# Kernel tuning notes

Hardware: AMD Instinct MI355X
Metric: run time of the kernel (lower is better)

Reference implementation:

```python
import jax, jax.numpy as jnp
import numpy as np

B, N, C = 8, 1024, 1024
H = 16
D = C // H  # head_dim = 64
SCALE = D ** -0.5


def setup_inputs() -> dict:
    key = jax.random.key(0)
    k1, k2, k3 = jax.random.split(key, 3)
    x = jax.random.normal(k1, (B, N, C), dtype=jnp.float32)
    w_qkv = jax.random.normal(k2, (3 * C, C), dtype=jnp.float32) * (C ** -0.5)
    w_proj = jax.random.normal(k3, (C, C), dtype=jnp.float32) * (C ** -0.5)
    b_proj = jnp.zeros((C,), dtype=jnp.float32)
    return {"x": x, "w_qkv": w_qkv, "w_proj": w_proj, "b_proj": b_proj}


def reference(x, w_qkv, w_proj, b_proj):
    Bx, Nx, Cx = x.shape
    # qkv: [B,N,3C] -> [3,B,H,N,D]
    qkv = jnp.einsum('bnc,oc->bno', x, w_qkv)
    qkv = qkv.reshape(Bx, Nx, 3, H, D).transpose(2, 0, 3, 1, 4)
    q, k, v = qkv[0], qkv[1], qkv[2]
    attn = jnp.einsum('bhnd,bhmd->bhnm', q, k) * SCALE  # [B,H,N,N]
    attn = jax.nn.softmax(attn, axis=-1)
    out = jnp.einsum('bhnm,bhmd->bhnd', attn, v)  # [B,H,N,D]
    out = out.transpose(0, 2, 1, 3).reshape(Bx, Nx, Cx)
    return jnp.einsum('bnc,oc->bno', out, w_proj) + b_proj
```

## Files before the change

### kernel.cpp

```cpp
#include <hip/hip_runtime.h>

typedef _Float16 half8 __attribute__((ext_vector_type(8)));
typedef _Float16 half4v __attribute__((ext_vector_type(4)));
typedef _Float16 half2v __attribute__((ext_vector_type(2)));
typedef float floatx4 __attribute__((ext_vector_type(4)));

#define AS3 __attribute__((address_space(3)))
#define AS1 __attribute__((address_space(1)))

__global__ __launch_bounds__(256) void cvt_f32_f16(const float* __restrict__ in,
                                                   _Float16* __restrict__ out, int n4) {
    int i = blockIdx.x * 256 + threadIdx.x;
    if (i >= n4) return;
    float4 v = ((const float4*)in)[i];
    half4v h = {(_Float16)v.x, (_Float16)v.y, (_Float16)v.z, (_Float16)v.w};
    ((half4v*)out)[i] = h;
}

__global__ __launch_bounds__(256, 3) void gemm_tn(
    const _Float16* __restrict__ A, const _Float16* __restrict__ B,
    _Float16* __restrict__ Ch, int ldc, _Float16* __restrict__ Ch2, int ldc2, int split,
    float* __restrict__ Cf, const float* __restrict__ bias,
    int M, int Nn, int K)
{
    __shared__ _Float16 sA[2][128 * 32];
    __shared__ _Float16 sB[2][128 * 32];
    const int tid  = threadIdx.x;
    const int lane = tid & 63, wave = tid >> 6;
    const int quad = lane >> 4, l16 = lane & 15;
    const int wr = wave >> 1, wc = wave & 1;
    const long m0 = (long)blockIdx.x * 128, n0 = (long)blockIdx.y * 128;

    const int srow = tid >> 2;
    const int sslot = ((tid & 3) ^ ((srow >> 1) & 3)) * 8;
    const int dlo = srow * 32 + sslot;
    const int dhi = (srow + 64) * 32 + sslot;
    const _Float16* gA0 = A + (m0 + srow) * (long)K + (tid & 3) * 8;
    const _Float16* gA1 = A + (m0 + srow + 64) * (long)K + (tid & 3) * 8;
    const _Float16* gB0 = B + (n0 + srow) * (long)K + (tid & 3) * 8;
    const _Float16* gB1 = B + (n0 + srow + 64) * (long)K + (tid & 3) * 8;

    const int swz = (l16 >> 1) & 3;
    const int aoff = ((quad ^ swz) * 8);

    floatx4 acc[4][4] = {};
    const int nk = K >> 5;

    half8 rA0 = *(const half8*)gA0, rA1 = *(const half8*)gA1;
    half8 rB0 = *(const half8*)gB0, rB1 = *(const half8*)gB1;
    *(half8*)&sA[0][dlo] = rA0; *(half8*)&sA[0][dhi] = rA1;
    *(half8*)&sB[0][dlo] = rB0; *(half8*)&sB[0][dhi] = rB1;

    for (int kk = 0; kk < nk; kk++) {
        const int cur = kk & 1;
        __syncthreads();
        const bool more = (kk + 1 < nk);
        if (more) {
            const long k0 = (long)(kk + 1) << 5;
            rA0 = *(const half8*)(gA0 + k0); rA1 = *(const half8*)(gA1 + k0);
            rB0 = *(const half8*)(gB0 + k0); rB1 = *(const half8*)(gB1 + k0);
        }

        const _Float16* cA = &sA[cur][0];
        const _Float16* cB = &sB[cur][0];
        half8 af[4], bf[4];
#pragma unroll
        for (int t = 0; t < 4; t++)
            af[t] = *(const half8*)&cA[(wr * 64 + t * 16 + l16) * 32 + aoff];
#pragma unroll
        for (int t = 0; t < 4; t++)
            bf[t] = *(const half8*)&cB[(wc * 64 + t * 16 + l16) * 32 + aoff];
#pragma unroll
        for (int tm = 0; tm < 4; tm++)
#pragma unroll
            for (int tn = 0; tn < 4; tn++)
                acc[tm][tn] = __builtin_amdgcn_mfma_f32_16x16x32_f16(af[tm], bf[tn], acc[tm][tn], 0, 0, 0);

        if (more) {
            _Float16* nA = &sA[cur ^ 1][0];
            _Float16* nB = &sB[cur ^ 1][0];
            *(half8*)&nA[dlo] = rA0; *(half8*)&nA[dhi] = rA1;
            *(half8*)&nB[dlo] = rB0; *(half8*)&nB[dhi] = rB1;
        }
    }

    const bool useC2 = (Cf == nullptr) && (n0 >= split);
#pragma unroll
    for (int tm = 0; tm < 4; tm++) {
        long row = m0 + wr * 64 + tm * 16 + quad * 4;
#pragma unroll
        for (int tn = 0; tn < 4; tn++) {
            long col = n0 + wc * 64 + tn * 16 + l16;
            float bv = bias ? bias[col] : 0.f;
#pragma unroll
            for (int r = 0; r < 4; r++) {
                float v = acc[tm][tn][r];
                if (Cf)        Cf[(row + r) * (long)Nn + col] = v + bv;
                else if (useC2) Ch2[(row + r) * (long)ldc2 + (col - split)] = (_Float16)v;
                else           Ch[(row + r) * (long)ldc + col] = (_Float16)v;
            }
        }
    }
}

__global__ __launch_bounds__(256) void transpose_v(const _Float16* __restrict__ vh,
                                                   _Float16* __restrict__ vt) {
    const int bh = blockIdx.x;
    const int b = bh >> 4, h = bh & 15;
    const int n0 = blockIdx.y * 64;
    const int d = threadIdx.x & 63;
    const int ng = threadIdx.x >> 6;
#pragma unroll
    for (int i = 0; i < 2; i++) {
        int nb = (ng + 4 * i) * 8;
        half8 vv;
#pragma unroll
        for (int j = 0; j < 8; j++)
            vv[j] = vh[(long)(b * 1024 + n0 + nb + j) * 1024 + h * 64 + d];
        *(half8*)&vt[((long)(bh * 64 + d)) * 1024 + n0 + nb] = vv;
    }
}

#define CSC 0.125f
__global__ __launch_bounds__(256, 4) void flash_attn(const _Float16* __restrict__ qk,
                                                     const _Float16* __restrict__ vt,
                                                     _Float16* __restrict__ out)
{
    const int bh = blockIdx.x, b = bh >> 4, h = bh & 15;
    const int n0 = blockIdx.y * 128;
    const int tid = threadIdx.x, lane = tid & 63, wave = tid >> 6;
    const int quad = lane >> 4, l16 = lane & 15;

    __shared__ _Float16 sK[64 * 72];
    __shared__ _Float16 sVT[64 * 72];
    __shared__ _Float16 sPT[4][32 * 72];

    half8 qf[2][2];
    const _Float16* qbase = qk + (long)(b * 1024 + n0 + wave * 32) * 2048 + h * 64;
#pragma unroll
    for (int t = 0; t < 2; t++)
#pragma unroll
        for (int s = 0; s < 2; s++)
            qf[t][s] = *(const half8*)(qbase + (long)(t * 16 + l16) * 2048 + s * 32 + quad * 8);

    const int srow = tid >> 3, scol8 = (tid & 7) * 8;
    const _Float16* kgb = qk + 1024 + h * 64 + scol8 + (long)(b * 1024 + srow) * 2048;
    const _Float16* vgb = vt + (long)(bh * 64 + srow) * 1024 + scol8;

    float m_[2] = {-1e30f, -1e30f}, l_[2] = {0.f, 0.f};
    floatx4 o[2][4] = {};

    for (int kt = 0; kt < 16; kt++) {
        const int kr0 = kt * 64;
        __syncthreads();
#pragma unroll
        for (int i = 0; i < 2; i++) {
            int r = srow + i * 32;
            *(half8*)&sK[r * 72 + scol8]  = *(const half8*)(kgb + (long)(kr0 + i * 32) * 2048);
            *(half8*)&sVT[r * 72 + scol8] = *(const half8*)(vgb + (long)(i * 32) * 1024 + kr0);
        }
        __syncthreads();

        floatx4 sacc[2][4] = {};
#pragma unroll
        for (int c = 0; c < 4; c++)
#pragma unroll
            for (int s = 0; s < 2; s++) {
                half8 kf = *(const half8*)&sK[(c * 16 + l16) * 72 + s * 32 + quad * 8];
                sacc[0][c] = __builtin_amdgcn_mfma_f32_16x16x32_f16(kf, qf[0][s], sacc[0][c], 0, 0, 0);
                sacc[1][c] = __builtin_amdgcn_mfma_f32_16x16x32_f16(kf, qf[1][s], sacc[1][c], 0, 0, 0);
            }

#pragma unroll
        for (int t = 0; t < 2; t++) {
            float mx = -1e30f;
#pragma unroll
            for (int c = 0; c < 4; c++)
#pragma unroll
                for (int r = 0; r < 4; r++) {
                    float v = sacc[t][c][r] * CSC;
                    sacc[t][c][r] = v;
                    mx = fmaxf(mx, v);
                }
            mx = fmaxf(mx, __shfl_xor(mx, 16));
            mx = fmaxf(mx, __shfl_xor(mx, 32));
            float mn = fmaxf(m_[t], mx);
            float al = __expf(m_[t] - mn);
            m_[t] = mn;
            float rs = 0.f;
#pragma unroll
            for (int c = 0; c < 4; c++)
#pragma unroll
                for (int r = 0; r < 4; r++) {
                    float p = __expf(sacc[t][c][r] - mn);
                    sacc[t][c][r] = p;
                    rs += p;
                }
            rs += __shfl_xor(rs, 16);
            rs += __shfl_xor(rs, 32);
            l_[t] = l_[t] * al + rs;
#pragma unroll
            for (int dt = 0; dt < 4; dt++) o[t][dt] *= al;
#pragma unroll
            for (int c = 0; c < 4; c++) {
                half2v p01 = {(_Float16)sacc[t][c][0], (_Float16)sacc[t][c][1]};
                half2v p23 = {(_Float16)sacc[t][c][2], (_Float16)sacc[t][c][3]};
                *(half2v*)&sPT[wave][(t * 16 + l16) * 72 + c * 16 + quad * 4]     = p01;
                *(half2v*)&sPT[wave][(t * 16 + l16) * 72 + c * 16 + quad * 4 + 2] = p23;
            }
        }

#pragma unroll
        for (int kk = 0; kk < 2; kk++) {
            half8 pf0 = *(const half8*)&sPT[wave][(l16) * 72 + kk * 32 + quad * 8];
            half8 pf1 = *(const half8*)&sPT[wave][(16 + l16) * 72 + kk * 32 + quad * 8];
#pragma unroll
            for (int dt = 0; dt < 4; dt++) {
                half8 vf = *(const half8*)&sVT[(dt * 16 + l16) * 72 + kk * 32 + quad * 8];
                o[0][dt] = __builtin_amdgcn_mfma_f32_16x16x32_f16(vf, pf0, o[0][dt], 0, 0, 0);
                o[1][dt] = __builtin_amdgcn_mfma_f32_16x16x32_f16(vf, pf1, o[1][dt], 0, 0, 0);
            }
        }
    }

#pragma unroll
    for (int t = 0; t < 2; t++) {
        float inv = 1.f / l_[t];
#pragma unroll
        for (int dt = 0; dt < 4; dt++) {
            floatx4 v = o[t][dt];
            half2v a = {(_Float16)(v[0] * inv), (_Float16)(v[1] * inv)};
            half2v c = {(_Float16)(v[2] * inv), (_Float16)(v[3] * inv)};
            *(half2v*)&sPT[wave][(t * 16 + l16) * 72 + dt * 16 + quad * 4]     = a;
            *(half2v*)&sPT[wave][(t * 16 + l16) * 72 + dt * 16 + quad * 4 + 2] = c;
        }
    }
    __syncthreads();
#pragma unroll
    for (int i = 0; i < 4; i++) {
        int ql = i * 8 + (lane >> 3);
        int c8 = (lane & 7) * 8;
        half8 vv = *(const half8*)&sPT[wave][ql * 72 + c8];
        *(half8*)(out + (long)(b * 1024 + n0 + wave * 32 + ql) * 1024 + h * 64 + c8) = vv;
    }
}

extern "C" void kernel_launch(void* const* d_in, const int* in_sizes, int n_in,
                              void* d_out, int out_size, void* d_ws, size_t ws_size,
                              hipStream_t stream) {
    const float* x      = (const float*)d_in[0];
    const float* w_qkv  = (const float*)d_in[1];
    const float* w_proj = (const float*)d_in[2];
    const float* b_proj = (const float*)d_in[3];

    char* ws = (char*)d_ws;
    _Float16* qkh    = (_Float16*)ws;
    _Float16* vh     = (_Float16*)(ws + 33554432);
    _Float16* xh     = (_Float16*)(ws + 50331648);
    _Float16* wqkvh  = (_Float16*)(ws + 67108864);
    _Float16* wprojh = (_Float16*)(ws + 73400320);
    _Float16* vT     = xh;
    _Float16* attnh  = vh;

    cvt_f32_f16<<<8192, 256, 0, stream>>>(x, xh, 8388608 / 4);
    cvt_f32_f16<<<3072, 256, 0, stream>>>(w_qkv, wqkvh, 3145728 / 4);
    cvt_f32_f16<<<1024, 256, 0, stream>>>(w_proj, wprojh, 1048576 / 4);

    gemm_tn<<<dim3(64, 24), 256, 0, stream>>>(xh, wqkvh, qkh, 2048, vh, 1024, 2048,
                                              nullptr, nullptr, 8192, 3072, 1024);
    transpose_v<<<dim3(128, 16), 256, 0, stream>>>(vh, vT);
    flash_attn<<<dim3(128, 8), 256, 0, stream>>>(qkh, vT, attnh);
    gemm_tn<<<dim3(64, 8), 256, 0, stream>>>(attnh, wprojh, nullptr, 0, nullptr, 0, 1 << 30,
                                             (float*)d_out, b_proj, 8192, 1024, 1024);
}
```

Measured before the change: 265.9 us.

## Load GEMM B fragments directly from global memory and fuse fp32-to-fp16 converts

The GEMM no longer stages the B (weight) tile through shared memory. Each wave loads its four B fragments straight from global memory into registers, prefetching one k-step ahead, which halves LDS traffic and LDS footprint. The cost is redundant global loads: the two waves that share a column block each fetch the same B data, and the per-lane 16-byte reads across rows are less coalesced. Separately, the three conversion kernels are merged into one launch to cut launch overhead.

```diff
diff --git a/kernel.cpp b/kernel.cpp
--- a/kernel.cpp
+++ b/kernel.cpp
@@ -8,13 +8,20 @@
 #define AS3 __attribute__((address_space(3)))
 #define AS1 __attribute__((address_space(1)))
 
-__global__ __launch_bounds__(256) void cvt_f32_f16(const float* __restrict__ in,
-                                                   _Float16* __restrict__ out, int n4) {
-    int i = blockIdx.x * 256 + threadIdx.x;
-    if (i >= n4) return;
-    float4 v = ((const float4*)in)[i];
+__global__ __launch_bounds__(256) void cvt_all(const float* __restrict__ x,
+                                               const float* __restrict__ wq,
+                                               const float* __restrict__ wp,
+                                               _Float16* __restrict__ xh,
+                                               _Float16* __restrict__ wqh,
+                                               _Float16* __restrict__ wph) {
+    long i = (long)blockIdx.x * 256 + threadIdx.x;
+    const float4* src; half4v* dst; long off;
+    if (i < 2097152)      { src = (const float4*)x;  dst = (half4v*)xh;  off = i; }
+    else if (i < 2883584) { src = (const float4*)wq; dst = (half4v*)wqh; off = i - 2097152; }
+    else                  { src = (const float4*)wp; dst = (half4v*)wph; off = i - 2883584; }
+    float4 v = src[off];
     half4v h = {(_Float16)v.x, (_Float16)v.y, (_Float16)v.z, (_Float16)v.w};
-    ((half4v*)out)[i] = h;
+    dst[off] = h;
 }
 
 __global__ __launch_bounds__(256, 3) void gemm_tn(
@@ -24,7 +31,6 @@
     int M, int Nn, int K)
 {
     __shared__ _Float16 sA[2][128 * 32];
-    __shared__ _Float16 sB[2][128 * 32];
     const int tid  = threadIdx.x;
     const int lane = tid & 63, wave = tid >> 6;
     const int quad = lane >> 4, l16 = lane & 15;
@@ -37,8 +43,9 @@
     const int dhi = (srow + 64) * 32 + sslot;
     const _Float16* gA0 = A + (m0 + srow) * (long)K + (tid & 3) * 8;
     const _Float16* gA1 = A + (m0 + srow + 64) * (long)K + (tid & 3) * 8;
-    const _Float16* gB0 = B + (n0 + srow) * (long)K + (tid & 3) * 8;
-    const _Float16* gB1 = B + (n0 + srow + 64) * (long)K + (tid & 3) * 8;
+
+    const _Float16* gB0 = B + (n0 + wc * 64 + l16) * (long)K + quad * 8;
+    const _Float16* gBf[4] = {gB0, gB0 + 16 * (long)K, gB0 + 32 * (long)K, gB0 + 48 * (long)K};
 
     const int swz = (l16 >> 1) & 3;
     const int aoff = ((quad ^ swz) * 8);
@@ -47,30 +54,29 @@
     const int nk = K >> 5;
 
     half8 rA0 = *(const half8*)gA0, rA1 = *(const half8*)gA1;
-    half8 rB0 = *(const half8*)gB0, rB1 = *(const half8*)gB1;
+    half8 bf[4], bn[4];
+#pragma unroll
+    for (int tn = 0; tn < 4; tn++) bf[tn] = *(const half8*)gBf[tn];
     *(half8*)&sA[0][dlo] = rA0; *(half8*)&sA[0][dhi] = rA1;
-    *(half8*)&sB[0][dlo] = rB0; *(half8*)&sB[0][dhi] = rB1;
 
     for (int kk = 0; kk < nk; kk++) {
         const int cur = kk & 1;
         __syncthreads();
         const bool more = (kk + 1 < nk);
         if (more) {
-            const long k0 = (long)(kk + 1) << 5;
-            rA0 = *(const half8*)(gA0 + k0); rA1 = *(const half8*)(gA1 + k0);
-            rB0 = *(const half8*)(gB0 + k0); rB1 = *(const half8*)(gB1 + k0);
+            const long k0n = (long)(kk + 1) << 5;
+            rA0 = *(const half8*)(gA0 + k0n);
+            rA1 = *(const half8*)(gA1 + k0n);
+#pragma unroll
+            for (int tn = 0; tn < 4; tn++) bn[tn] = *(const half8*)(gBf[tn] + k0n);
         }
 
         const _Float16* cA = &sA[cur][0];
-        const _Float16* cB = &sB[cur][0];
-        half8 af[4], bf[4];
+        half8 af[4];
 #pragma unroll
         for (int t = 0; t < 4; t++)
             af[t] = *(const half8*)&cA[(wr * 64 + t * 16 + l16) * 32 + aoff];
 #pragma unroll
-        for (int t = 0; t < 4; t++)
-            bf[t] = *(const half8*)&cB[(wc * 64 + t * 16 + l16) * 32 + aoff];
-#pragma unroll
         for (int tm = 0; tm < 4; tm++)
 #pragma unroll
             for (int tn = 0; tn < 4; tn++)
@@ -78,9 +84,10 @@
 
         if (more) {
             _Float16* nA = &sA[cur ^ 1][0];
-            _Float16* nB = &sB[cur ^ 1][0];
-            *(half8*)&nA[dlo] = rA0; *(half8*)&nA[dhi] = rA1;
-            *(half8*)&nB[dlo] = rB0; *(half8*)&nB[dhi] = rB1;
+            *(half8*)&nA[dlo] = rA0;
+            *(half8*)&nA[dhi] = rA1;
+#pragma unroll
+            for (int tn = 0; tn < 4; tn++) bf[tn] = bn[tn];
         }
     }
 
@@ -262,9 +269,7 @@
     _Float16* vT     = xh;
     _Float16* attnh  = vh;
 
-    cvt_f32_f16<<<8192, 256, 0, stream>>>(x, xh, 8388608 / 4);
-    cvt_f32_f16<<<3072, 256, 0, stream>>>(w_qkv, wqkvh, 3145728 / 4);
-    cvt_f32_f16<<<1024, 256, 0, stream>>>(w_proj, wprojh, 1048576 / 4);
+    cvt_all<<<12288, 256, 0, stream>>>(x, w_qkv, w_proj, xh, wqkvh, wprojh);
 
     gemm_tn<<<dim3(64, 24), 256, 0, stream>>>(xh, wqkvh, qkh, 2048, vh, 1024, 2048,
                                               nullptr, nullptr, 8192, 3072, 1024);
```

Result: slower. 321.1 us (+20.8%).

## Fuse V transpose into QKV GEMM epilogue and merge conversion kernels

Applied to the files above, without the earlier changes.

The QKV GEMM epilogue now writes the V columns directly in transposed [b,h,d,n] layout, which removes the separate transpose_v kernel and its extra read and write of V. The three fp32-to-fp16 conversion launches become one kernel. The GEMM occupancy hint rises from 3 to 4 waves per SIMD, and LDS stores of P and O use 4-wide half vectors instead of pairs. The epilogue's V stores are strided across rows, which may coalesce poorly, and the higher occupancy hint may cause register spills.

```diff
diff --git a/kernel.cpp b/kernel.cpp
--- a/kernel.cpp
+++ b/kernel.cpp
@@ -8,18 +8,25 @@
 #define AS3 __attribute__((address_space(3)))
 #define AS1 __attribute__((address_space(1)))
 
-__global__ __launch_bounds__(256) void cvt_f32_f16(const float* __restrict__ in,
-                                                   _Float16* __restrict__ out, int n4) {
-    int i = blockIdx.x * 256 + threadIdx.x;
-    if (i >= n4) return;
-    float4 v = ((const float4*)in)[i];
+__global__ __launch_bounds__(256) void cvt_all(const float* __restrict__ x,
+                                               const float* __restrict__ wq,
+                                               const float* __restrict__ wp,
+                                               _Float16* __restrict__ xh,
+                                               _Float16* __restrict__ wqh,
+                                               _Float16* __restrict__ wph) {
+    long i = (long)blockIdx.x * 256 + threadIdx.x;
+    const float4* src; half4v* dst; long off;
+    if (i < 2097152)      { src = (const float4*)x;  dst = (half4v*)xh;  off = i; }
+    else if (i < 2883584) { src = (const float4*)wq; dst = (half4v*)wqh; off = i - 2097152; }
+    else                  { src = (const float4*)wp; dst = (half4v*)wph; off = i - 2883584; }
+    float4 v = src[off];
     half4v h = {(_Float16)v.x, (_Float16)v.y, (_Float16)v.z, (_Float16)v.w};
-    ((half4v*)out)[i] = h;
-}
-
-__global__ __launch_bounds__(256, 3) void gemm_tn(
+    dst[off] = h;
+}
+
+__global__ __launch_bounds__(256, 4) void gemm_tn(
     const _Float16* __restrict__ A, const _Float16* __restrict__ B,
-    _Float16* __restrict__ Ch, int ldc, _Float16* __restrict__ Ch2, int ldc2, int split,
+    _Float16* __restrict__ Ch, int ldc, _Float16* __restrict__ Vt, int split,
     float* __restrict__ Cf, const float* __restrict__ bias,
     int M, int Nn, int K)
 {
@@ -84,40 +91,30 @@
         }
     }
 
-    const bool useC2 = (Cf == nullptr) && (n0 >= split);
 #pragma unroll
     for (int tm = 0; tm < 4; tm++) {
         long row = m0 + wr * 64 + tm * 16 + quad * 4;
 #pragma unroll
         for (int tn = 0; tn < 4; tn++) {
             long col = n0 + wc * 64 + tn * 16 + l16;
-            float bv = bias ? bias[col] : 0.f;
-#pragma unroll
-            for (int r = 0; r < 4; r++) {
-                float v = acc[tm][tn][r];
-                if (Cf)        Cf[(row + r) * (long)Nn + col] = v + bv;
-                else if (useC2) Ch2[(row + r) * (long)ldc2 + (col - split)] = (_Float16)v;
-                else           Ch[(row + r) * (long)ldc + col] = (_Float16)v;
-            }
-        }
-    }
-}
-
-__global__ __launch_bounds__(256) void transpose_v(const _Float16* __restrict__ vh,
-                                                   _Float16* __restrict__ vt) {
-    const int bh = blockIdx.x;
-    const int b = bh >> 4, h = bh & 15;
-    const int n0 = blockIdx.y * 64;
-    const int d = threadIdx.x & 63;
-    const int ng = threadIdx.x >> 6;
-#pragma unroll
-    for (int i = 0; i < 2; i++) {
-        int nb = (ng + 4 * i) * 8;
-        half8 vv;
-#pragma unroll
-        for (int j = 0; j < 8; j++)
-            vv[j] = vh[(long)(b * 1024 + n0 + nb + j) * 1024 + h * 64 + d];
-        *(half8*)&vt[((long)(bh * 64 + d)) * 1024 + n0 + nb] = vv;
+            if (Cf) {
+                float bv = bias ? bias[col] : 0.f;
+#pragma unroll
+                for (int r = 0; r < 4; r++)
+                    Cf[(row + r) * (long)Nn + col] = acc[tm][tn][r] + bv;
+            } else if (col >= split) {
+                long cv = col - split;
+                long vrow = ((row >> 10) * 16 + (cv >> 6)) * 64 + (cv & 63);
+                long nn = row & 1023;
+                half4v pv = {(_Float16)acc[tm][tn][0], (_Float16)acc[tm][tn][1],
+                             (_Float16)acc[tm][tn][2], (_Float16)acc[tm][tn][3]};
+                *(half4v*)&Vt[vrow * 1024 + nn] = pv;
+            } else {
+#pragma unroll
+                for (int r = 0; r < 4; r++)
+                    Ch[(row + r) * (long)ldc + col] = (_Float16)acc[tm][tn][r];
+            }
+        }
     }
 }
 
@@ -203,10 +200,9 @@
             for (int dt = 0; dt < 4; dt++) o[t][dt] *= al;
 #pragma unroll
             for (int c = 0; c < 4; c++) {
-                half2v p01 = {(_Float16)sacc[t][c][0], (_Float16)sacc[t][c][1]};
-                half2v p23 = {(_Float16)sacc[t][c][2], (_Float16)sacc[t][c][3]};
-                *(half2v*)&sPT[wave][(t * 16 + l16) * 72 + c * 16 + quad * 4]     = p01;
-                *(half2v*)&sPT[wave][(t * 16 + l16) * 72 + c * 16 + quad * 4 + 2] = p23;
+                half4v p = {(_Float16)sacc[t][c][0], (_Float16)sacc[t][c][1],
+                            (_Float16)sacc[t][c][2], (_Float16)sacc[t][c][3]};
+                *(half4v*)&sPT[wave][(t * 16 + l16) * 72 + c * 16 + quad * 4] = p;
             }
         }
 
@@ -229,10 +225,9 @@
 #pragma unroll
         for (int dt = 0; dt < 4; dt++) {
             floatx4 v = o[t][dt];
-            half2v a = {(_Float16)(v[0] * inv), (_Float16)(v[1] * inv)};
-            half2v c = {(_Float16)(v[2] * inv), (_Float16)(v[3] * inv)};
-            *(half2v*)&sPT[wave][(t * 16 + l16) * 72 + dt * 16 + quad * 4]     = a;
-            *(half2v*)&sPT[wave][(t * 16 + l16) * 72 + dt * 16 + quad * 4 + 2] = c;
+            half4v a = {(_Float16)(v[0] * inv), (_Float16)(v[1] * inv),
+                        (_Float16)(v[2] * inv), (_Float16)(v[3] * inv)};
+            *(half4v*)&sPT[wave][(t * 16 + l16) * 72 + dt * 16 + quad * 4] = a;
         }
     }
     __syncthreads();
@@ -255,21 +250,17 @@
 
     char* ws = (char*)d_ws;
     _Float16* qkh    = (_Float16*)ws;
-    _Float16* vh     = (_Float16*)(ws + 33554432);
+    _Float16* vT     = (_Float16*)(ws + 33554432);
     _Float16* xh     = (_Float16*)(ws + 50331648);
     _Float16* wqkvh  = (_Float16*)(ws + 67108864);
     _Float16* wprojh = (_Float16*)(ws + 73400320);
-    _Float16* vT     = xh;
-    _Float16* attnh  = vh;
-
-    cvt_f32_f16<<<8192, 256, 0, stream>>>(x, xh, 8388608 / 4);
-    cvt_f32_f16<<<3072, 256, 0, stream>>>(w_qkv, wqkvh, 3145728 / 4);
-    cvt_f32_f16<<<1024, 256, 0, stream>>>(w_proj, wprojh, 1048576 / 4);
-
-    gemm_tn<<<dim3(64, 24), 256, 0, stream>>>(xh, wqkvh, qkh, 2048, vh, 1024, 2048,
+    _Float16* attnh  = xh;
+
+    cvt_all<<<12288, 256, 0, stream>>>(x, w_qkv, w_proj, xh, wqkvh, wprojh);
+
+    gemm_tn<<<dim3(64, 24), 256, 0, stream>>>(xh, wqkvh, qkh, 2048, vT, 2048,
                                               nullptr, nullptr, 8192, 3072, 1024);
-    transpose_v<<<dim3(128, 16), 256, 0, stream>>>(vh, vT);
     flash_attn<<<dim3(128, 8), 256, 0, stream>>>(qkh, vT, attnh);
-    gemm_tn<<<dim3(64, 8), 256, 0, stream>>>(attnh, wprojh, nullptr, 0, nullptr, 0, 1 << 30,
+    gemm_tn<<<dim3(64, 8), 256, 0, stream>>>(attnh, wprojh, nullptr, 0, nullptr, 1 << 30,
                                              (float*)d_out, b_proj, 8192, 1024, 1024);
 }
```

Result: faster. 248.3 us (-6.6%).
